# Kernel optimization log

Hardware: AMD Instinct MI355X
Metric: run time of the kernel (lower is better)

The kernel has to match this reference:

```python
import jax, jax.numpy as jnp
import numpy as np

N_NODES = 100000
N_EDGES = 1600000
IN_CH = 128
HID = 128
OUT_CH = 16
N_GRAPHS = 64


def setup_inputs() -> dict:
    key = jax.random.key(0)
    ks = jax.random.split(key, 8)
    x = jax.random.normal(ks[0], (N_NODES, IN_CH), dtype=jnp.float32)
    edge_index = jax.random.randint(ks[1], (2, N_EDGES), 0, N_NODES, dtype=jnp.int64)
    batch = jnp.sort(jax.random.randint(ks[2], (N_NODES,), 0, N_GRAPHS, dtype=jnp.int64))
    s1 = 1.0 / np.sqrt(IN_CH)
    s2 = 1.0 / np.sqrt(HID)
    W1 = jax.random.uniform(ks[3], (IN_CH, HID), jnp.float32, -s1, s1)
    b1 = jnp.zeros((HID,), jnp.float32)
    W2 = jax.random.uniform(ks[4], (HID, HID), jnp.float32, -s2, s2)
    b2 = jnp.zeros((HID,), jnp.float32)
    Wfc = jax.random.uniform(ks[5], (HID, OUT_CH), jnp.float32, -s2, s2)
    bfc = jax.random.uniform(ks[6], (OUT_CH,), jnp.float32, -s2, s2)
    return {"x": x, "W1": W1, "b1": b1, "W2": W2, "b2": b2,
            "Wfc": Wfc, "bfc": bfc, "edge_index": edge_index, "batch": batch}


def _gcn_conv(x, W, b, src, dst, deg_inv_sqrt, deg_inv):
    # GCNConv with self-loops: out = D^-1/2 (A+I) D^-1/2 (x W) + b
    h = x @ W                                   # [N, H]
    norm = deg_inv_sqrt[src] * deg_inv_sqrt[dst]  # [E]
    agg = jax.ops.segment_sum(h[src] * norm[:, None], dst, num_segments=N_NODES)
    # self-loop term: deg_inv_sqrt[i]^2 * h[i]
    return agg + h * deg_inv[:, None] + b


def reference(x, W1, b1, W2, b2, Wfc, bfc, edge_index, batch):
    src, dst = edge_index[0], edge_index[1]
    # degree including self-loop
    deg = jax.ops.segment_sum(jnp.ones((N_EDGES,), jnp.float32), dst, num_segments=N_NODES) + 1.0
    deg_inv_sqrt = jax.lax.rsqrt(deg)
    deg_inv = 1.0 / deg
    h = jax.nn.relu(_gcn_conv(x, W1, b1, src, dst, deg_inv_sqrt, deg_inv))
    h = jax.nn.relu(_gcn_conv(h, W2, b2, src, dst, deg_inv_sqrt, deg_inv))
    # global mean pool over graphs
    sums = jax.ops.segment_sum(h, batch, num_segments=N_GRAPHS)          # [G, H]
    counts = jax.ops.segment_sum(jnp.ones((N_NODES,), jnp.float32), batch, num_segments=N_GRAPHS)
    pooled = sums / jnp.maximum(counts, 1.0)[:, None]
    return pooled @ Wfc + bfc
```

## Files before the change

kernel.cpp:

```cpp
#include <hip/hip_runtime.h>
#include <math.h>

#define NN 100000
#define NE 1600000
#define CH 128
#define OUTC 16
#define NG 64

#define CBSH 9
#define NCB 196
#define CHK 8192
#define MAXB 12288
#define PS 8

typedef __attribute__((ext_vector_type(8))) short bf16x8;
typedef __attribute__((ext_vector_type(4))) float f32x4;

__device__ __forceinline__ unsigned short f2bf(float f) {
    union { float f; unsigned u; } v; v.f = f;
    unsigned r = v.u + 0x7FFF + ((v.u >> 16) & 1);
    return (unsigned short)(r >> 16);
}
__device__ __forceinline__ float bflo(unsigned u) {
    union { unsigned u; float f; } v; v.u = u << 16; return v.f;
}
__device__ __forceinline__ float bfhi(unsigned u) {
    union { unsigned u; float f; } v; v.u = u & 0xffff0000u; return v.f;
}

__global__ void k_init0(int* __restrict__ bcnt) {
    int i = blockIdx.x * 256 + threadIdx.x;
    if (i < NCB) bcnt[i] = 0;
}

__global__ __launch_bounds__(1024) void k_hist(const int* __restrict__ dst, int* __restrict__ bcnt) {
    __shared__ int h[NCB];
    int t = threadIdx.x;
    if (t < NCB) h[t] = 0;
    __syncthreads();
    int base = blockIdx.x * CHK;
#pragma unroll
    for (int i = 0; i < 8; i++) {
        int e = base + i * 1024 + t;
        if (e < NE) atomicAdd(&h[dst[e] >> CBSH], 1);
    }
    __syncthreads();
    if (t < NCB && h[t]) atomicAdd(&bcnt[t], h[t]);
}

__global__ __launch_bounds__(1024) void k_bscan(const int* __restrict__ bcnt, int* __restrict__ ebase,
                        int* __restrict__ gfill, float* __restrict__ pooled) {
    __shared__ int s[256];
    int t = threadIdx.x;
    if (t < 256) s[t] = (t < NCB) ? bcnt[t] : 0;
    __syncthreads();
    for (int off = 1; off < 256; off <<= 1) {
        int v = 0;
        if (t < 256 && t >= off) v = s[t - off];
        __syncthreads();
        if (t < 256) s[t] += v;
        __syncthreads();
    }
    if (t == 0) ebase[0] = 0;
    if (t < NCB) { ebase[t + 1] = s[t]; gfill[t] = 0; }
    for (int i = t; i < NG * CH; i += 1024) pooled[i] = 0.f;
}

__global__ __launch_bounds__(1024) void k_passA(const int* __restrict__ src, const int* __restrict__ dst,
                        const int* __restrict__ ebase, int* __restrict__ gfill,
                        unsigned* __restrict__ ebuf) {
    __shared__ unsigned lbuf[CHK];
    __shared__ int hcnt[NCB];
    __shared__ int hbase[256];
    __shared__ int goff[NCB];
    int t = threadIdx.x;
    if (t < NCB) hcnt[t] = 0;
    __syncthreads();
    int base = blockIdx.x * CHK;
    int cb[8], slot[8]; unsigned pk[8];
#pragma unroll
    for (int i = 0; i < 8; i++) {
        int e = base + i * 1024 + t;
        cb[i] = -1;
        if (e < NE) {
            int d = dst[e], s = src[e];
            cb[i] = d >> CBSH;
            pk[i] = ((unsigned)s << CBSH) | (unsigned)(d & 511);
            slot[i] = atomicAdd(&hcnt[cb[i]], 1);
        }
    }
    __syncthreads();
    if (t < 256) hbase[t] = (t < NCB) ? hcnt[t] : 0;
    __syncthreads();
    for (int off = 1; off < 256; off <<= 1) {
        int v = 0;
        if (t < 256 && t >= off) v = hbase[t - off];
        __syncthreads();
        if (t < 256) hbase[t] += v;
        __syncthreads();
    }
    if (t < NCB) {
        int c = hcnt[t];
        int g = c ? atomicAdd(&gfill[t], c) : 0;
        goff[t] = ebase[t] + g - (hbase[t] - c);
    }
    __syncthreads();
#pragma unroll
    for (int i = 0; i < 8; i++) {
        if (cb[i] >= 0) lbuf[hbase[cb[i]] - hcnt[cb[i]] + slot[i]] = pk[i];
    }
    __syncthreads();
    int total = min(NE - base, CHK);
    for (int p = t; p < total; p += 1024) {
        unsigned v = lbuf[p];
        int lo = 0, hi = NCB - 1;
        while (lo < hi) { int mid = (lo + hi) >> 1; if (hbase[mid] > p) hi = mid; else lo = mid + 1; }
        ebuf[goff[lo] + p] = v;
    }
}

__global__ __launch_bounds__(1024) void k_passB(const unsigned* __restrict__ ebuf, const int* __restrict__ ebase,
                        int* __restrict__ degi, int* __restrict__ rowst,
                        float* __restrict__ dis, int* __restrict__ csr) {
    __shared__ int cnt[512];
    __shared__ int nbase[512];
    __shared__ int fill[512];
    __shared__ int stage[MAXB];
    int t = threadIdx.x;
    int cb = blockIdx.x;
    int nb0 = cb << CBSH;
    int ncnt = min(512, NN - nb0);
    int e0 = ebase[cb], e1 = ebase[cb + 1];
    if (t < 512) { cnt[t] = 0; fill[t] = 0; }
    __syncthreads();
    for (int e = e0 + t; e < e1; e += 1024)
        atomicAdd(&cnt[ebuf[e] & 511], 1);
    __syncthreads();
    if (t < 512) nbase[t] = cnt[t];
    __syncthreads();
    for (int off = 1; off < 512; off <<= 1) {
        int v = 0;
        if (t < 512 && t >= off) v = nbase[t - off];
        __syncthreads();
        if (t < 512) nbase[t] += v;
        __syncthreads();
    }
    for (int e = e0 + t; e < e1; e += 1024) {
        unsigned v = ebuf[e];
        int local = v & 511;
        int s = atomicAdd(&fill[local], 1);
        stage[nbase[local] - cnt[local] + s] = (int)(v >> CBSH);
    }
    __syncthreads();
    int total = e1 - e0;
    for (int p = t; p < total; p += 1024) csr[e0 + p] = stage[p];
    if (t < ncnt) {
        int c = cnt[t];
        degi[nb0 + t] = c;
        rowst[nb0 + t] = e0 + nbase[t] - c;
        dis[nb0 + t] = rsqrtf((float)c + 1.0f);
    }
}

__global__ void k_gptr(const int* __restrict__ batch, int* __restrict__ gptr) {
    int n = blockIdx.x * 256 + threadIdx.x;
    if (n >= NN) return;
    int b = batch[n];
    int prev = (n == 0) ? -1 : batch[n - 1];
    for (int g = prev + 1; g <= b; g++) gptr[g] = n;
    if (n == NN - 1) {
        for (int g = b + 1; g <= NG; g++) gptr[g] = NN;
    }
}

__global__ void k_cast(const float* __restrict__ in, unsigned short* __restrict__ out, int n4) {
    int i = blockIdx.x * 256 + threadIdx.x;
    if (i >= n4) return;
    float4 v = *(const float4*)&in[(size_t)i * 4];
    ushort4 o;
    o.x = f2bf(v.x); o.y = f2bf(v.y); o.z = f2bf(v.z); o.w = f2bf(v.w);
    *(ushort4*)&out[(size_t)i * 4] = o;
}

__global__ void k_castW(const float* __restrict__ W1, const float* __restrict__ W2,
                        unsigned short* __restrict__ wt1, unsigned short* __restrict__ wt2) {
    int i = blockIdx.x * 256 + threadIdx.x;
    if (i < CH * CH) {
        int k = i >> 7, n = i & 127;
        wt1[n * CH + k] = f2bf(W1[i]);
    } else if (i < 2 * CH * CH) {
        int j = i - CH * CH;
        int k = j >> 7, n = j & 127;
        wt2[n * CH + k] = f2bf(W2[j]);
    }
}

__launch_bounds__(256, 2)
__global__ void k_gemm_mfma(const unsigned short* __restrict__ A,
                            const unsigned short* __restrict__ WT,
                            const float* __restrict__ dis,
                            unsigned short* __restrict__ out) {
    int tid = threadIdx.x;
    int wave = tid >> 6, lane = tid & 63;
    int quad = lane >> 4, l16 = lane & 15;

    int row = blockIdx.x * 64 + wave * 16 + l16;
    int rowc = row < NN ? row : NN - 1;

    const unsigned short* arow = A + (size_t)rowc * CH + quad * 8;
    bf16x8 af0 = *(const bf16x8*)(arow);
    bf16x8 af1 = *(const bf16x8*)(arow + 32);
    bf16x8 af2 = *(const bf16x8*)(arow + 64);
    bf16x8 af3 = *(const bf16x8*)(arow + 96);

    f32x4 acc[8];
#pragma unroll
    for (int t = 0; t < 8; t++) acc[t] = (f32x4){0.f, 0.f, 0.f, 0.f};

#pragma unroll
    for (int t = 0; t < 8; t++) {
        const unsigned short* wcol = WT + (size_t)(t * 16 + l16) * CH + quad * 8;
        bf16x8 b0 = *(const bf16x8*)(wcol);
        bf16x8 b1 = *(const bf16x8*)(wcol + 32);
        bf16x8 b2 = *(const bf16x8*)(wcol + 64);
        bf16x8 b3 = *(const bf16x8*)(wcol + 96);
        acc[t] = __builtin_amdgcn_mfma_f32_16x16x32_bf16(af0, b0, acc[t], 0, 0, 0);
        acc[t] = __builtin_amdgcn_mfma_f32_16x16x32_bf16(af1, b1, acc[t], 0, 0, 0);
        acc[t] = __builtin_amdgcn_mfma_f32_16x16x32_bf16(af2, b2, acc[t], 0, 0, 0);
        acc[t] = __builtin_amdgcn_mfma_f32_16x16x32_bf16(af3, b3, acc[t], 0, 0, 0);
    }

    int rbase = blockIdx.x * 64 + wave * 16 + quad * 4;
#pragma unroll
    for (int r = 0; r < 4; r++) {
        int orow = rbase + r;
        if (orow < NN) {
            float d = dis[orow];
#pragma unroll
            for (int t = 0; t < 8; t++) {
                out[(size_t)orow * CH + t * 16 + l16] = f2bf(acc[t][r] * d);
            }
        }
    }
}

__global__ void k_agg(const unsigned short* __restrict__ ht, const int* __restrict__ rowst,
                      const int* __restrict__ degi, const int* __restrict__ csr,
                      const float* __restrict__ dis, const float* __restrict__ bias,
                      unsigned short* __restrict__ out) {
    int wave = threadIdx.x >> 6;
    int lane = threadIdx.x & 63;
    int n = blockIdx.x * 4 + wave;
    if (n >= NN) return;
    const unsigned* base = (const unsigned*)ht;
    unsigned sv = base[(size_t)n * 64 + lane];
    float a0 = bflo(sv), a1 = bfhi(sv);
    float b0 = 0.f, b1 = 0.f, c0 = 0.f, c1 = 0.f, d0 = 0.f, d1 = 0.f;
    int start = rowst[n], c = degi[n];
    int j = 0;
    for (; j + 3 < c; j += 4) {
        int s0 = csr[start + j];
        int s1 = csr[start + j + 1];
        int s2 = csr[start + j + 2];
        int s3 = csr[start + j + 3];
        unsigned v0 = base[(size_t)s0 * 64 + lane];
        unsigned v1 = base[(size_t)s1 * 64 + lane];
        unsigned v2 = base[(size_t)s2 * 64 + lane];
        unsigned v3 = base[(size_t)s3 * 64 + lane];
        a0 += bflo(v0); a1 += bfhi(v0);
        b0 += bflo(v1); b1 += bfhi(v1);
        c0 += bflo(v2); c1 += bfhi(v2);
        d0 += bflo(v3); d1 += bfhi(v3);
    }
    for (; j < c; j++) {
        unsigned v0 = base[(size_t)csr[start + j] * 64 + lane];
        a0 += bflo(v0); a1 += bfhi(v0);
    }
    float sx = (a0 + b0) + (c0 + d0);
    float sy = (a1 + b1) + (c1 + d1);
    float d = dis[n];
    float bb0 = bias[lane * 2], bb1 = bias[lane * 2 + 1];
    float ox = fmaxf(fmaf(d, sx, bb0), 0.f);
    float oy = fmaxf(fmaf(d, sy, bb1), 0.f);
    unsigned pk = ((unsigned)f2bf(oy) << 16) | (unsigned)f2bf(ox);
    ((unsigned*)out)[(size_t)n * 64 + lane] = pk;
}

__global__ __launch_bounds__(512) void k_pool2(const unsigned short* __restrict__ h,
                                               const int* __restrict__ gptr,
                                               float* __restrict__ pooled) {
    int g = blockIdx.x >> 3;
    int s = blockIdx.x & 7;
    int gs = gptr[g], ge = gptr[g + 1];
    int len = ge - gs;
    int i0 = gs + (int)(((long long)len * s) >> 3);
    int i1 = gs + (int)(((long long)len * (s + 1)) >> 3);
    int t = threadIdx.x;
    int pr = t & 63;
    int ro = t >> 6;
    const unsigned* base = (const unsigned*)h;
    float s0 = 0.f, s1 = 0.f;
    for (int n = i0 + ro; n < i1; n += 8) {
        unsigned v = base[(size_t)n * 64 + pr];
        s0 += bflo(v); s1 += bfhi(v);
    }
    __shared__ float red[2][8][64];
    red[0][ro][pr] = s0; red[1][ro][pr] = s1;
    __syncthreads();
    for (int off = 4; off >= 1; off >>= 1) {
        if (ro < off) {
            red[0][ro][pr] += red[0][ro + off][pr];
            red[1][ro][pr] += red[1][ro + off][pr];
        }
        __syncthreads();
    }
    if (ro == 0) {
        atomicAdd(&pooled[g * CH + pr * 2],     red[0][0][pr]);
        atomicAdd(&pooled[g * CH + pr * 2 + 1], red[1][0][pr]);
    }
}

__global__ void k_final(const float* __restrict__ pooled, const int* __restrict__ gptr,
                        const float* __restrict__ Wfc, const float* __restrict__ bfc,
                        float* __restrict__ out) {
    int idx = blockIdx.x * 256 + threadIdx.x;
    if (idx >= NG * OUTC) return;
    int g = idx >> 4, o = idx & 15;
    float c = (float)(gptr[g + 1] - gptr[g]);
    float inv = 1.0f / fmaxf(c, 1.0f);
    float s = 0.f;
    for (int k = 0; k < CH; k++) s += pooled[g * CH + k] * Wfc[k * OUTC + o];
    out[idx] = fmaf(s, inv, bfc[o]);
}

extern "C" void kernel_launch(void* const* d_in, const int* in_sizes, int n_in,
                              void* d_out, int out_size, void* d_ws, size_t ws_size,
                              hipStream_t stream) {
    (void)in_sizes; (void)n_in; (void)out_size; (void)ws_size;
    const float* x   = (const float*)d_in[0];
    const float* W1  = (const float*)d_in[1];
    const float* b1  = (const float*)d_in[2];
    const float* W2  = (const float*)d_in[3];
    const float* b2  = (const float*)d_in[4];
    const float* Wfc = (const float*)d_in[5];
    const float* bfc = (const float*)d_in[6];
    const int* ei    = (const int*)d_in[7];
    const int* batch = (const int*)d_in[8];
    const int* esrc = ei;
    const int* edst = ei + NE;
    float* out = (float*)d_out;

    char* w = (char*)d_ws;
    unsigned short* xb   = (unsigned short*)w; w += (size_t)NN * CH * 2;
    unsigned short* bufA = (unsigned short*)w; w += (size_t)NN * CH * 2;
    unsigned short* bufB = (unsigned short*)w; w += (size_t)NN * CH * 2;
    unsigned short* wt1  = (unsigned short*)w; w += (size_t)CH * CH * 2;
    unsigned short* wt2  = (unsigned short*)w; w += (size_t)CH * CH * 2;
    unsigned* ebuf = (unsigned*)w; w += (size_t)NE * 4;
    int* csr    = (int*)w;    w += (size_t)NE * 4;
    int* degi   = (int*)w;    w += (size_t)NN * 4;
    int* rowst  = (int*)w;    w += (size_t)NN * 4;
    float* dis  = (float*)w;  w += (size_t)NN * 4;
    int* bcnt   = (int*)w;    w += NCB * 4;
    int* ebase  = (int*)w;    w += (NCB + 1) * 4;
    int* gfill  = (int*)w;    w += NCB * 4;
    int* gptr   = (int*)w;    w += (NG + 1) * 4;
    float* pooled = (float*)w; w += (size_t)NG * CH * 4;

    const int histBlocks = (NE + CHK - 1) / CHK;

    k_init0<<<1, 256, 0, stream>>>(bcnt);
    k_hist<<<histBlocks, 1024, 0, stream>>>(edst, bcnt);
    k_bscan<<<1, 1024, 0, stream>>>(bcnt, ebase, gfill, pooled);
    k_passA<<<histBlocks, 1024, 0, stream>>>(esrc, edst, ebase, gfill, ebuf);
    k_passB<<<NCB, 1024, 0, stream>>>(ebuf, ebase, degi, rowst, dis, csr);
    k_gptr<<<(NN + 255) / 256, 256, 0, stream>>>(batch, gptr);

    k_cast<<<(NN * CH / 4 + 255) / 256, 256, 0, stream>>>(x, xb, NN * CH / 4);
    k_castW<<<(2 * CH * CH + 255) / 256, 256, 0, stream>>>(W1, W2, wt1, wt2);

    const int gemmBlocks = (NN + 63) / 64;

    k_gemm_mfma<<<gemmBlocks, 256, 0, stream>>>(xb, wt1, dis, bufA);
    k_agg<<<NN / 4, 256, 0, stream>>>(bufA, rowst, degi, csr, dis, b1, bufB);
    k_gemm_mfma<<<gemmBlocks, 256, 0, stream>>>(bufB, wt2, dis, bufA);
    k_agg<<<NN / 4, 256, 0, stream>>>(bufA, rowst, degi, csr, dis, b2, bufB);

    k_pool2<<<NG * PS, 512, 0, stream>>>(bufB, gptr, pooled);
    k_final<<<(NG * OUTC + 255) / 256, 256, 0, stream>>>(pooled, gptr, Wfc, bfc, out);
}
```

Baseline: 377.8 us.

## Fuse fp32-to-bf16 cast into first GEMM, widen GEMM tiles, deepen aggregation unroll

The separate cast kernel for x is removed. The first GEMM now reads fp32 rows and converts them to bf16 in registers, which drops a full write and re-read of a 25 MB intermediate and one launch. Each GEMM wave now handles 32 rows instead of 16, so every loaded weight fragment feeds two MFMAs and weight traffic per row halves, at the cost of more registers. The aggregation kernel unrolls the neighbor gather to 8 independent loads with 8 accumulator pairs, and makes the row start and degree wave-uniform via readfirstlane, to raise memory-level parallelism.

```diff
diff --git a/kernel.cpp b/kernel.cpp
--- a/kernel.cpp
+++ b/kernel.cpp
@@ -173,15 +173,6 @@
     }
 }
 
-__global__ void k_cast(const float* __restrict__ in, unsigned short* __restrict__ out, int n4) {
-    int i = blockIdx.x * 256 + threadIdx.x;
-    if (i >= n4) return;
-    float4 v = *(const float4*)&in[(size_t)i * 4];
-    ushort4 o;
-    o.x = f2bf(v.x); o.y = f2bf(v.y); o.z = f2bf(v.z); o.w = f2bf(v.w);
-    *(ushort4*)&out[(size_t)i * 4] = o;
-}
-
 __global__ void k_castW(const float* __restrict__ W1, const float* __restrict__ W2,
                         unsigned short* __restrict__ wt1, unsigned short* __restrict__ wt2) {
     int i = blockIdx.x * 256 + threadIdx.x;
@@ -195,27 +186,48 @@
     }
 }
 
+template<bool F32IN>
 __launch_bounds__(256, 2)
-__global__ void k_gemm_mfma(const unsigned short* __restrict__ A,
-                            const unsigned short* __restrict__ WT,
-                            const float* __restrict__ dis,
-                            unsigned short* __restrict__ out) {
+__global__ void k_gemm(const void* __restrict__ Av,
+                       const unsigned short* __restrict__ WT,
+                       const float* __restrict__ dis,
+                       unsigned short* __restrict__ out) {
     int tid = threadIdx.x;
     int wave = tid >> 6, lane = tid & 63;
     int quad = lane >> 4, l16 = lane & 15;
 
-    int row = blockIdx.x * 64 + wave * 16 + l16;
-    int rowc = row < NN ? row : NN - 1;
-
-    const unsigned short* arow = A + (size_t)rowc * CH + quad * 8;
-    bf16x8 af0 = *(const bf16x8*)(arow);
-    bf16x8 af1 = *(const bf16x8*)(arow + 32);
-    bf16x8 af2 = *(const bf16x8*)(arow + 64);
-    bf16x8 af3 = *(const bf16x8*)(arow + 96);
-
-    f32x4 acc[8];
-#pragma unroll
-    for (int t = 0; t < 8; t++) acc[t] = (f32x4){0.f, 0.f, 0.f, 0.f};
+    int rbase = blockIdx.x * 128 + wave * 32;
+
+    bf16x8 af[2][4];
+#pragma unroll
+    for (int s = 0; s < 2; s++) {
+        int row = rbase + s * 16 + l16;
+        if (row >= NN) row = NN - 1;
+        if (F32IN) {
+            const float* arow = (const float*)Av + (size_t)row * CH + quad * 8;
+#pragma unroll
+            for (int ks = 0; ks < 4; ks++) {
+                float4 lo = *(const float4*)(arow + ks * 32);
+                float4 hi = *(const float4*)(arow + ks * 32 + 4);
+                union { bf16x8 v; unsigned short u[8]; } tmp;
+                tmp.u[0] = f2bf(lo.x); tmp.u[1] = f2bf(lo.y);
+                tmp.u[2] = f2bf(lo.z); tmp.u[3] = f2bf(lo.w);
+                tmp.u[4] = f2bf(hi.x); tmp.u[5] = f2bf(hi.y);
+                tmp.u[6] = f2bf(hi.z); tmp.u[7] = f2bf(hi.w);
+                af[s][ks] = tmp.v;
+            }
+        } else {
+            const unsigned short* arow = (const unsigned short*)Av + (size_t)row * CH + quad * 8;
+#pragma unroll
+            for (int ks = 0; ks < 4; ks++) af[s][ks] = *(const bf16x8*)(arow + ks * 32);
+        }
+    }
+
+    f32x4 acc[2][8];
+#pragma unroll
+    for (int s = 0; s < 2; s++)
+#pragma unroll
+        for (int t = 0; t < 8; t++) acc[s][t] = (f32x4){0.f, 0.f, 0.f, 0.f};
 
 #pragma unroll
     for (int t = 0; t < 8; t++) {
@@ -224,21 +236,26 @@
         bf16x8 b1 = *(const bf16x8*)(wcol + 32);
         bf16x8 b2 = *(const bf16x8*)(wcol + 64);
         bf16x8 b3 = *(const bf16x8*)(wcol + 96);
-        acc[t] = __builtin_amdgcn_mfma_f32_16x16x32_bf16(af0, b0, acc[t], 0, 0, 0);
-        acc[t] = __builtin_amdgcn_mfma_f32_16x16x32_bf16(af1, b1, acc[t], 0, 0, 0);
-        acc[t] = __builtin_amdgcn_mfma_f32_16x16x32_bf16(af2, b2, acc[t], 0, 0, 0);
-        acc[t] = __builtin_amdgcn_mfma_f32_16x16x32_bf16(af3, b3, acc[t], 0, 0, 0);
-    }
-
-    int rbase = blockIdx.x * 64 + wave * 16 + quad * 4;
-#pragma unroll
-    for (int r = 0; r < 4; r++) {
-        int orow = rbase + r;
-        if (orow < NN) {
-            float d = dis[orow];
-#pragma unroll
-            for (int t = 0; t < 8; t++) {
-                out[(size_t)orow * CH + t * 16 + l16] = f2bf(acc[t][r] * d);
+#pragma unroll
+        for (int s = 0; s < 2; s++) {
+            acc[s][t] = __builtin_amdgcn_mfma_f32_16x16x32_bf16(af[s][0], b0, acc[s][t], 0, 0, 0);
+            acc[s][t] = __builtin_amdgcn_mfma_f32_16x16x32_bf16(af[s][1], b1, acc[s][t], 0, 0, 0);
+            acc[s][t] = __builtin_amdgcn_mfma_f32_16x16x32_bf16(af[s][2], b2, acc[s][t], 0, 0, 0);
+            acc[s][t] = __builtin_amdgcn_mfma_f32_16x16x32_bf16(af[s][3], b3, acc[s][t], 0, 0, 0);
+        }
+    }
+
+#pragma unroll
+    for (int s = 0; s < 2; s++) {
+#pragma unroll
+        for (int r = 0; r < 4; r++) {
+            int orow = rbase + s * 16 + quad * 4 + r;
+            if (orow < NN) {
+                float d = dis[orow];
+#pragma unroll
+                for (int t = 0; t < 8; t++) {
+                    out[(size_t)orow * CH + t * 16 + l16] = f2bf(acc[s][t][r] * d);
+                }
             }
         }
     }
@@ -254,34 +271,35 @@
     if (n >= NN) return;
     const unsigned* base = (const unsigned*)ht;
     unsigned sv = base[(size_t)n * 64 + lane];
-    float a0 = bflo(sv), a1 = bfhi(sv);
-    float b0 = 0.f, b1 = 0.f, c0 = 0.f, c1 = 0.f, d0 = 0.f, d1 = 0.f;
-    int start = rowst[n], c = degi[n];
+    float a0[8], a1[8];
+    a0[0] = bflo(sv); a1[0] = bfhi(sv);
+#pragma unroll
+    for (int u = 1; u < 8; u++) { a0[u] = 0.f; a1[u] = 0.f; }
+    int start = __builtin_amdgcn_readfirstlane(rowst[n]);
+    int c = __builtin_amdgcn_readfirstlane(degi[n]);
     int j = 0;
-    for (; j + 3 < c; j += 4) {
-        int s0 = csr[start + j];
-        int s1 = csr[start + j + 1];
-        int s2 = csr[start + j + 2];
-        int s3 = csr[start + j + 3];
-        unsigned v0 = base[(size_t)s0 * 64 + lane];
-        unsigned v1 = base[(size_t)s1 * 64 + lane];
-        unsigned v2 = base[(size_t)s2 * 64 + lane];
-        unsigned v3 = base[(size_t)s3 * 64 + lane];
-        a0 += bflo(v0); a1 += bfhi(v0);
-        b0 += bflo(v1); b1 += bfhi(v1);
-        c0 += bflo(v2); c1 += bfhi(v2);
-        d0 += bflo(v3); d1 += bfhi(v3);
+    for (; j + 7 < c; j += 8) {
+        int idx[8];
+#pragma unroll
+        for (int u = 0; u < 8; u++) idx[u] = csr[start + j + u];
+        unsigned v[8];
+#pragma unroll
+        for (int u = 0; u < 8; u++) v[u] = base[(size_t)idx[u] * 64 + lane];
+#pragma unroll
+        for (int u = 0; u < 8; u++) { a0[u] += bflo(v[u]); a1[u] += bfhi(v[u]); }
     }
     for (; j < c; j++) {
         unsigned v0 = base[(size_t)csr[start + j] * 64 + lane];
-        a0 += bflo(v0); a1 += bfhi(v0);
-    }
-    float sx = (a0 + b0) + (c0 + d0);
-    float sy = (a1 + b1) + (c1 + d1);
+        a0[j & 7] += bflo(v0); a1[j & 7] += bfhi(v0);
+    }
+#pragma unroll
+    for (int off = 4; off >= 1; off >>= 1)
+#pragma unroll
+        for (int u = 0; u < off; u++) { a0[u] += a0[u + off]; a1[u] += a1[u + off]; }
     float d = dis[n];
     float bb0 = bias[lane * 2], bb1 = bias[lane * 2 + 1];
-    float ox = fmaxf(fmaf(d, sx, bb0), 0.f);
-    float oy = fmaxf(fmaf(d, sy, bb1), 0.f);
+    float ox = fmaxf(fmaf(d, a0[0], bb0), 0.f);
+    float oy = fmaxf(fmaf(d, a1[0], bb1), 0.f);
     unsigned pk = ((unsigned)f2bf(oy) << 16) | (unsigned)f2bf(ox);
     ((unsigned*)out)[(size_t)n * 64 + lane] = pk;
 }
@@ -351,7 +369,6 @@
     float* out = (float*)d_out;
 
     char* w = (char*)d_ws;
-    unsigned short* xb   = (unsigned short*)w; w += (size_t)NN * CH * 2;
     unsigned short* bufA = (unsigned short*)w; w += (size_t)NN * CH * 2;
     unsigned short* bufB = (unsigned short*)w; w += (size_t)NN * CH * 2;
     unsigned short* wt1  = (unsigned short*)w; w += (size_t)CH * CH * 2;
@@ -368,6 +385,7 @@
     float* pooled = (float*)w; w += (size_t)NG * CH * 4;
 
     const int histBlocks = (NE + CHK - 1) / CHK;
+    const int gemmBlocks = (NN + 127) / 128;
 
     k_init0<<<1, 256, 0, stream>>>(bcnt);
     k_hist<<<histBlocks, 1024, 0, stream>>>(edst, bcnt);
@@ -376,14 +394,11 @@
     k_passB<<<NCB, 1024, 0, stream>>>(ebuf, ebase, degi, rowst, dis, csr);
     k_gptr<<<(NN + 255) / 256, 256, 0, stream>>>(batch, gptr);
 
-    k_cast<<<(NN * CH / 4 + 255) / 256, 256, 0, stream>>>(x, xb, NN * CH / 4);
     k_castW<<<(2 * CH * CH + 255) / 256, 256, 0, stream>>>(W1, W2, wt1, wt2);
 
-    const int gemmBlocks = (NN + 63) / 64;
-
-    k_gemm_mfma<<<gemmBlocks, 256, 0, stream>>>(xb, wt1, dis, bufA);
+    k_gemm<true><<<gemmBlocks, 256, 0, stream>>>(x, wt1, dis, bufA);
     k_agg<<<NN / 4, 256, 0, stream>>>(bufA, rowst, degi, csr, dis, b1, bufB);
-    k_gemm_mfma<<<gemmBlocks, 256, 0, stream>>>(bufB, wt2, dis, bufA);
+    k_gemm<false><<<gemmBlocks, 256, 0, stream>>>(bufB, wt2, dis, bufA);
     k_agg<<<NN / 4, 256, 0, stream>>>(bufA, rowst, degi, csr, dis, b2, bufB);
 
     k_pool2<<<NG * PS, 512, 0, stream>>>(bufB, gptr, pooled);
```

Result: faster. 334.0 us (-11.6%).
